# Optimization experiments

Hardware: AMD Instinct MI355X
Metric: run time of the kernel (lower is better)

## Reference

```python
import jax, jax.numpy as jnp
import numpy as np

NUM_CAMERAS = 16
IN_SIZE = 256
OUT_SIZE = 128
BATCH = 8192


def setup_inputs() -> dict:
    key = jax.random.key(0)
    k1, k2, k3, k4 = jax.random.split(key, 4)
    x = jax.random.normal(k1, (BATCH, IN_SIZE), dtype=jnp.float32)
    cam = jax.random.randint(k2, (BATCH,), 0, NUM_CAMERAS, dtype=jnp.int64)
    # Per-camera Linear params, torch-style init U(-1/sqrt(in), 1/sqrt(in))
    bound = 1.0 / np.sqrt(IN_SIZE)
    W = jax.random.uniform(k3, (NUM_CAMERAS, OUT_SIZE, IN_SIZE), dtype=jnp.float32, minval=-bound, maxval=bound)
    b = jax.random.uniform(k4, (NUM_CAMERAS, OUT_SIZE), dtype=jnp.float32, minval=-bound, maxval=bound)
    return {"x": x, "cam": cam, "W": W, "b": b}


def reference(x, cam, W, b):
    # Per-sample expert linear: y_b = W[cam_b] @ x_b + b[cam_b], then sigmoid.
    Wg = W[cam]            # [B, out, in] gathered per-sample weights
    bg = b[cam]            # [B, out]
    y = jnp.einsum('bi,boi->bo', x, Wg) + bg
    return jax.nn.sigmoid(y)
```

## Files before the change

kernel.cpp:

```cpp
#include <hip/hip_runtime.h>
#include <hip/hip_bf16.h>

#define NCAM   16
#define IN     256
#define OUT    128
#define BATCH  8192
#define NSLICE 16
#define SLICE  (BATCH / NSLICE)
#define XPAD   8
#define XROW   (IN + XPAD)

typedef __attribute__((ext_vector_type(8))) short  bfx8;
typedef __attribute__((ext_vector_type(4))) short  bfx4;
typedef __attribute__((ext_vector_type(4))) float  fx4;

__device__ inline short f2bf(float f) {
    __hip_bfloat16 h = __float2bfloat16(f);
    return *reinterpret_cast<short*>(&h);
}

__device__ inline float sigmoidf(float v) {
    return 1.0f / (1.0f + __expf(-v));
}

__global__ __launch_bounds__(256) void fc_expert_kernel(
    const float* __restrict__ x,
    const int*   __restrict__ cam,
    const float* __restrict__ W,
    const float* __restrict__ bias,
    float*       __restrict__ out)
{
    __shared__ int   s_list[SLICE];
    __shared__ int   s_m;
    __shared__ short __align__(16) s_x[16 * XROW];

    const int slice = blockIdx.x;
    const int c     = blockIdx.y;
    const int tid   = threadIdx.x;
    const int lane  = tid & 63;
    const int w     = tid >> 6;
    const int base  = slice * SLICE;

    const int oq   = lane & 15;
    const int quad = lane >> 4;

    if (tid < 64) {
        int cnt = 0;
        for (int i = 0; i < SLICE; i += 64) {
            int g = base + i + lane;
            bool f = (cam[g] == c);
            unsigned long long mask = __ballot(f);
            int pre = __popcll(mask & ((1ull << lane) - 1ull));
            if (f) s_list[cnt + pre] = g;
            cnt += __popcll(mask);
        }
        if (lane == 0) s_m = cnt;
    }

    bfx8 bfrag[2][8];
    #pragma unroll
    for (int t = 0; t < 2; ++t) {
        const int o = w * 32 + t * 16 + oq;
        const float* wrow = W + (size_t)(c * OUT + o) * IN + quad * 8;
        #pragma unroll
        for (int kk = 0; kk < 8; ++kk) {
            fx4 f0 = *(const fx4*)(wrow + kk * 32);
            fx4 f1 = *(const fx4*)(wrow + kk * 32 + 4);
            bfx8 s;
            s[0] = f2bf(f0[0]); s[1] = f2bf(f0[1]); s[2] = f2bf(f0[2]); s[3] = f2bf(f0[3]);
            s[4] = f2bf(f1[0]); s[5] = f2bf(f1[1]); s[6] = f2bf(f1[2]); s[7] = f2bf(f1[3]);
            bfrag[t][kk] = s;
        }
    }
    const float b0 = bias[c * OUT + w * 32 + oq];
    const float b1 = bias[c * OUT + w * 32 + 16 + oq];

    __syncthreads();
    const int m = s_m;

    for (int cb = 0; cb < m; cb += 16) {
        #pragma unroll
        for (int rr = 0; rr < 4; ++rr) {
            int row = rr * 4 + w;
            int li  = cb + row;
            bfx4 sv;
            if (li < m) {
                int g = s_list[li];
                fx4 v = *(const fx4*)(x + (size_t)g * IN + lane * 4);
                sv[0] = f2bf(v[0]); sv[1] = f2bf(v[1]); sv[2] = f2bf(v[2]); sv[3] = f2bf(v[3]);
            } else {
                sv[0] = 0; sv[1] = 0; sv[2] = 0; sv[3] = 0;
            }
            *(bfx4*)(s_x + row * XROW + lane * 4) = sv;
        }
        __syncthreads();

        fx4 acc0 = {0.f, 0.f, 0.f, 0.f};
        fx4 acc1 = {0.f, 0.f, 0.f, 0.f};
        #pragma unroll
        for (int kk = 0; kk < 8; ++kk) {
            bfx8 a = *(const bfx8*)(s_x + oq * XROW + kk * 32 + quad * 8);
            acc0 = __builtin_amdgcn_mfma_f32_16x16x32_bf16(a, bfrag[0][kk], acc0, 0, 0, 0);
            acc1 = __builtin_amdgcn_mfma_f32_16x16x32_bf16(a, bfrag[1][kk], acc1, 0, 0, 0);
        }

        #pragma unroll
        for (int r = 0; r < 4; ++r) {
            int srow = quad * 4 + r;
            if (cb + srow < m) {
                int g = s_list[cb + srow];
                float* op = out + (size_t)g * OUT + w * 32 + oq;
                op[0]  = sigmoidf(acc0[r] + b0);
                op[16] = sigmoidf(acc1[r] + b1);
            }
        }
        __syncthreads();
    }
}

extern "C" void kernel_launch(void* const* d_in, const int* in_sizes, int n_in,
                              void* d_out, int out_size, void* d_ws, size_t ws_size,
                              hipStream_t stream) {
    const float* x    = (const float*)d_in[0];
    const int*   cam  = (const int*)d_in[1];
    const float* W    = (const float*)d_in[2];
    const float* bias = (const float*)d_in[3];
    float* out = (float*)d_out;

    dim3 grid(NSLICE, NCAM);
    fc_expert_kernel<<<grid, 256, 0, stream>>>(x, cam, W, bias, out);
}
```

Baseline: 76.87 us.

## Split output columns across grid z, double slices, parallelize camera scan

Grid grows from 16x16 to 32x16x2 blocks: batch slices are halved and each block handles only 64 of the 128 output columns. Each wave now computes a single MFMA tile. The camera-match scan now uses all four waves with a per-wave count exchanged through shared memory, instead of one wave looping. Weight loads are issued before the scan to overlap latency. This targets low occupancy and the serial scan, at the cost of each x row being loaded and converted twice, once per output half.

```diff
diff --git a/kernel.cpp b/kernel.cpp
--- a/kernel.cpp
+++ b/kernel.cpp
@@ -5,8 +5,9 @@
 #define IN     256
 #define OUT    128
 #define BATCH  8192
-#define NSLICE 16
+#define NSLICE 32
 #define SLICE  (BATCH / NSLICE)
+#define OHALF  64
 #define XPAD   8
 #define XROW   (IN + XPAD)
 
@@ -23,7 +24,7 @@
     return 1.0f / (1.0f + __expf(-v));
 }
 
-__global__ __launch_bounds__(256) void fc_expert_kernel(
+__global__ __launch_bounds__(256, 2) void fc_expert_kernel(
     const float* __restrict__ x,
     const int*   __restrict__ cam,
     const float* __restrict__ W,
@@ -31,11 +32,12 @@
     float*       __restrict__ out)
 {
     __shared__ int   s_list[SLICE];
-    __shared__ int   s_m;
+    __shared__ int   s_cnt[4];
     __shared__ short __align__(16) s_x[16 * XROW];
 
     const int slice = blockIdx.x;
     const int c     = blockIdx.y;
+    const int obase = blockIdx.z * OHALF;
     const int tid   = threadIdx.x;
     const int lane  = tid & 63;
     const int w     = tid >> 6;
@@ -44,39 +46,40 @@
     const int oq   = lane & 15;
     const int quad = lane >> 4;
 
-    if (tid < 64) {
-        int cnt = 0;
-        for (int i = 0; i < SLICE; i += 64) {
-            int g = base + i + lane;
-            bool f = (cam[g] == c);
-            unsigned long long mask = __ballot(f);
-            int pre = __popcll(mask & ((1ull << lane) - 1ull));
-            if (f) s_list[cnt + pre] = g;
-            cnt += __popcll(mask);
-        }
-        if (lane == 0) s_m = cnt;
+    const int g0   = base + w * 64 + lane;
+    const int myc  = cam[g0];
+
+    const int o = obase + w * 16 + oq;
+    const float* wrow = W + (size_t)(c * OUT + o) * IN + quad * 8;
+    fx4 wt[16];
+    #pragma unroll
+    for (int kk = 0; kk < 8; ++kk) {
+        wt[2 * kk]     = *(const fx4*)(wrow + kk * 32);
+        wt[2 * kk + 1] = *(const fx4*)(wrow + kk * 32 + 4);
     }
+    const float bo = bias[c * OUT + o];
 
-    bfx8 bfrag[2][8];
+    const bool f = (myc == c);
+    const unsigned long long mask = __ballot(f);
+    if (lane == 0) s_cnt[w] = __popcll(mask);
+    __syncthreads();
+    int off = 0;
     #pragma unroll
-    for (int t = 0; t < 2; ++t) {
-        const int o = w * 32 + t * 16 + oq;
-        const float* wrow = W + (size_t)(c * OUT + o) * IN + quad * 8;
-        #pragma unroll
-        for (int kk = 0; kk < 8; ++kk) {
-            fx4 f0 = *(const fx4*)(wrow + kk * 32);
-            fx4 f1 = *(const fx4*)(wrow + kk * 32 + 4);
-            bfx8 s;
-            s[0] = f2bf(f0[0]); s[1] = f2bf(f0[1]); s[2] = f2bf(f0[2]); s[3] = f2bf(f0[3]);
-            s[4] = f2bf(f1[0]); s[5] = f2bf(f1[1]); s[6] = f2bf(f1[2]); s[7] = f2bf(f1[3]);
-            bfrag[t][kk] = s;
-        }
+    for (int ww = 0; ww < 4; ++ww) off += (ww < w) ? s_cnt[ww] : 0;
+    const int m = s_cnt[0] + s_cnt[1] + s_cnt[2] + s_cnt[3];
+    const int pre = __popcll(mask & ((1ull << lane) - 1ull));
+    if (f) s_list[off + pre] = g0;
+
+    bfx8 bfrag[8];
+    #pragma unroll
+    for (int kk = 0; kk < 8; ++kk) {
+        fx4 f0 = wt[2 * kk], f1 = wt[2 * kk + 1];
+        bfx8 s;
+        s[0] = f2bf(f0[0]); s[1] = f2bf(f0[1]); s[2] = f2bf(f0[2]); s[3] = f2bf(f0[3]);
+        s[4] = f2bf(f1[0]); s[5] = f2bf(f1[1]); s[6] = f2bf(f1[2]); s[7] = f2bf(f1[3]);
+        bfrag[kk] = s;
     }
-    const float b0 = bias[c * OUT + w * 32 + oq];
-    const float b1 = bias[c * OUT + w * 32 + 16 + oq];
-
     __syncthreads();
-    const int m = s_m;
 
     for (int cb = 0; cb < m; cb += 16) {
         #pragma unroll
@@ -95,13 +98,11 @@
         }
         __syncthreads();
 
-        fx4 acc0 = {0.f, 0.f, 0.f, 0.f};
-        fx4 acc1 = {0.f, 0.f, 0.f, 0.f};
+        fx4 acc = {0.f, 0.f, 0.f, 0.f};
         #pragma unroll
         for (int kk = 0; kk < 8; ++kk) {
             bfx8 a = *(const bfx8*)(s_x + oq * XROW + kk * 32 + quad * 8);
-            acc0 = __builtin_amdgcn_mfma_f32_16x16x32_bf16(a, bfrag[0][kk], acc0, 0, 0, 0);
-            acc1 = __builtin_amdgcn_mfma_f32_16x16x32_bf16(a, bfrag[1][kk], acc1, 0, 0, 0);
+            acc = __builtin_amdgcn_mfma_f32_16x16x32_bf16(a, bfrag[kk], acc, 0, 0, 0);
         }
 
         #pragma unroll
@@ -109,9 +110,7 @@
             int srow = quad * 4 + r;
             if (cb + srow < m) {
                 int g = s_list[cb + srow];
-                float* op = out + (size_t)g * OUT + w * 32 + oq;
-                op[0]  = sigmoidf(acc0[r] + b0);
-                op[16] = sigmoidf(acc1[r] + b1);
+                out[(size_t)g * OUT + o] = sigmoidf(acc[r] + bo);
             }
         }
         __syncthreads();
@@ -127,6 +126,6 @@
     const float* bias = (const float*)d_in[3];
     float* out = (float*)d_out;
 
-    dim3 grid(NSLICE, NCAM);
+    dim3 grid(NSLICE, NCAM, 2);
     fc_expert_kernel<<<grid, 256, 0, stream>>>(x, cam, W, bias, out);
 }
```

After: 74.01 us. -3.7%, faster.

## Bucket samples per camera globally with atomics and tile GEMM over compacted lists

Applied to the files above, without the earlier changes.

Replaces the per-slice ballot scan inside the GEMM kernel with a separate zero pass and an atomic compaction pass that builds a global per-camera index list. The GEMM grid then launches 32-row tiles per camera, and any tile beyond the camera's count exits early. Each block stages the full camera weight matrix in LDS as bf16 and loads x rows directly from global memory into registers, which removes the per-iteration barriers. The cost is two extra kernel launches, atomic contention on 16 counters, and a large grid of mostly empty blocks that still launch.

```diff
diff --git a/kernel.cpp b/kernel.cpp
--- a/kernel.cpp
+++ b/kernel.cpp
@@ -5,14 +5,14 @@
 #define IN     256
 #define OUT    128
 #define BATCH  8192
-#define NSLICE 16
-#define SLICE  (BATCH / NSLICE)
-#define XPAD   8
-#define XROW   (IN + XPAD)
+#define CAP    8192
+#define MT     32
+#define NTILE  (CAP / MT)
+#define XROWW  (IN + 8)
 
-typedef __attribute__((ext_vector_type(8))) short  bfx8;
-typedef __attribute__((ext_vector_type(4))) short  bfx4;
-typedef __attribute__((ext_vector_type(4))) float  fx4;
+typedef short bfx8 __attribute__((ext_vector_type(8)));
+typedef short bfx4 __attribute__((ext_vector_type(4)));
+typedef float fx4  __attribute__((ext_vector_type(4)));
 
 __device__ inline short f2bf(float f) {
     __hip_bfloat16 h = __float2bfloat16(f);
@@ -23,98 +23,94 @@
     return 1.0f / (1.0f + __expf(-v));
 }
 
-__global__ __launch_bounds__(256) void fc_expert_kernel(
+__global__ void zero_cnt_kernel(int* __restrict__ cnt) {
+    if (threadIdx.x < NCAM) cnt[threadIdx.x] = 0;
+}
+
+__global__ void compact_kernel(const int* __restrict__ cam,
+                               int* __restrict__ cnt,
+                               int* __restrict__ list) {
+    int g = blockIdx.x * 256 + threadIdx.x;
+    int c = cam[g];
+    int slot = atomicAdd(&cnt[c], 1);
+    list[c * CAP + slot] = g;
+}
+
+__global__ __launch_bounds__(256, 2) void gemm_kernel(
     const float* __restrict__ x,
-    const int*   __restrict__ cam,
     const float* __restrict__ W,
     const float* __restrict__ bias,
+    const int*   __restrict__ cnt,
+    const int*   __restrict__ list,
     float*       __restrict__ out)
 {
-    __shared__ int   s_list[SLICE];
-    __shared__ int   s_m;
-    __shared__ short __align__(16) s_x[16 * XROW];
+    __shared__ short __align__(16) s_w[OUT * XROWW];
 
-    const int slice = blockIdx.x;
-    const int c     = blockIdx.y;
-    const int tid   = threadIdx.x;
-    const int lane  = tid & 63;
-    const int w     = tid >> 6;
-    const int base  = slice * SLICE;
+    const int t = blockIdx.x;
+    const int c = blockIdx.y;
+    const int m_all = cnt[c];
+    const int base  = t * MT;
+    if (base >= m_all) return;
+    const int m = min(MT, m_all - base);
 
+    const int tid  = threadIdx.x;
+    const int lane = tid & 63;
+    const int w    = tid >> 6;
     const int oq   = lane & 15;
     const int quad = lane >> 4;
 
-    if (tid < 64) {
-        int cnt = 0;
-        for (int i = 0; i < SLICE; i += 64) {
-            int g = base + i + lane;
-            bool f = (cam[g] == c);
-            unsigned long long mask = __ballot(f);
-            int pre = __popcll(mask & ((1ull << lane) - 1ull));
-            if (f) s_list[cnt + pre] = g;
-            cnt += __popcll(mask);
-        }
-        if (lane == 0) s_m = cnt;
-    }
-
-    bfx8 bfrag[2][8];
-    #pragma unroll
-    for (int t = 0; t < 2; ++t) {
-        const int o = w * 32 + t * 16 + oq;
-        const float* wrow = W + (size_t)(c * OUT + o) * IN + quad * 8;
+    {
+        const float* wp = W + (size_t)c * OUT * IN;
         #pragma unroll
-        for (int kk = 0; kk < 8; ++kk) {
-            fx4 f0 = *(const fx4*)(wrow + kk * 32);
-            fx4 f1 = *(const fx4*)(wrow + kk * 32 + 4);
-            bfx8 s;
-            s[0] = f2bf(f0[0]); s[1] = f2bf(f0[1]); s[2] = f2bf(f0[2]); s[3] = f2bf(f0[3]);
-            s[4] = f2bf(f1[0]); s[5] = f2bf(f1[1]); s[6] = f2bf(f1[2]); s[7] = f2bf(f1[3]);
-            bfrag[t][kk] = s;
+        for (int i = 0; i < 32; ++i) {
+            const int row = w * 32 + i;
+            fx4 v = *(const fx4*)(wp + (size_t)row * IN + lane * 4);
+            bfx4 sv;
+            sv[0] = f2bf(v[0]); sv[1] = f2bf(v[1]); sv[2] = f2bf(v[2]); sv[3] = f2bf(v[3]);
+            *(bfx4*)(s_w + row * XROWW + lane * 4) = sv;
         }
     }
     const float b0 = bias[c * OUT + w * 32 + oq];
     const float b1 = bias[c * OUT + w * 32 + 16 + oq];
+    __syncthreads();
 
-    __syncthreads();
-    const int m = s_m;
+    const int* lst = list + c * CAP + base;
 
     for (int cb = 0; cb < m; cb += 16) {
+        const int li = cb + oq;
+        const int g  = lst[min(li, m - 1)];
+        const float* xr = x + (size_t)g * IN + quad * 8;
+        bfx8 afrag[8];
         #pragma unroll
-        for (int rr = 0; rr < 4; ++rr) {
-            int row = rr * 4 + w;
-            int li  = cb + row;
-            bfx4 sv;
-            if (li < m) {
-                int g = s_list[li];
-                fx4 v = *(const fx4*)(x + (size_t)g * IN + lane * 4);
-                sv[0] = f2bf(v[0]); sv[1] = f2bf(v[1]); sv[2] = f2bf(v[2]); sv[3] = f2bf(v[3]);
-            } else {
-                sv[0] = 0; sv[1] = 0; sv[2] = 0; sv[3] = 0;
-            }
-            *(bfx4*)(s_x + row * XROW + lane * 4) = sv;
+        for (int kk = 0; kk < 8; ++kk) {
+            fx4 a0 = *(const fx4*)(xr + kk * 32);
+            fx4 a1 = *(const fx4*)(xr + kk * 32 + 4);
+            bfx8 s;
+            s[0] = f2bf(a0[0]); s[1] = f2bf(a0[1]); s[2] = f2bf(a0[2]); s[3] = f2bf(a0[3]);
+            s[4] = f2bf(a1[0]); s[5] = f2bf(a1[1]); s[6] = f2bf(a1[2]); s[7] = f2bf(a1[3]);
+            afrag[kk] = s;
         }
-        __syncthreads();
 
         fx4 acc0 = {0.f, 0.f, 0.f, 0.f};
         fx4 acc1 = {0.f, 0.f, 0.f, 0.f};
         #pragma unroll
         for (int kk = 0; kk < 8; ++kk) {
-            bfx8 a = *(const bfx8*)(s_x + oq * XROW + kk * 32 + quad * 8);
-            acc0 = __builtin_amdgcn_mfma_f32_16x16x32_bf16(a, bfrag[0][kk], acc0, 0, 0, 0);
-            acc1 = __builtin_amdgcn_mfma_f32_16x16x32_bf16(a, bfrag[1][kk], acc1, 0, 0, 0);
+            bfx8 bv0 = *(const bfx8*)(s_w + (w * 32 + oq) * XROWW + kk * 32 + quad * 8);
+            bfx8 bv1 = *(const bfx8*)(s_w + (w * 32 + 16 + oq) * XROWW + kk * 32 + quad * 8);
+            acc0 = __builtin_amdgcn_mfma_f32_16x16x32_bf16(afrag[kk], bv0, acc0, 0, 0, 0);
+            acc1 = __builtin_amdgcn_mfma_f32_16x16x32_bf16(afrag[kk], bv1, acc1, 0, 0, 0);
         }
 
         #pragma unroll
         for (int r = 0; r < 4; ++r) {
-            int srow = quad * 4 + r;
+            const int srow = quad * 4 + r;
             if (cb + srow < m) {
-                int g = s_list[cb + srow];
-                float* op = out + (size_t)g * OUT + w * 32 + oq;
+                const int gs = lst[cb + srow];
+                float* op = out + (size_t)gs * OUT + w * 32 + oq;
                 op[0]  = sigmoidf(acc0[r] + b0);
                 op[16] = sigmoidf(acc1[r] + b1);
             }
         }
-        __syncthreads();
     }
 }
 
@@ -127,6 +123,11 @@
     const float* bias = (const float*)d_in[3];
     float* out = (float*)d_out;
 
-    dim3 grid(NSLICE, NCAM);
-    fc_expert_kernel<<<grid, 256, 0, stream>>>(x, cam, W, bias, out);
+    int* cnt  = (int*)d_ws;
+    int* list = (int*)((char*)d_ws + 256);
+
+    zero_cnt_kernel<<<1, 64, 0, stream>>>(cnt);
+    compact_kernel<<<BATCH / 256, 256, 0, stream>>>(cam, cnt, list);
+    dim3 grid(NTILE, NCAM);
+    gemm_kernel<<<grid, 256, 0, stream>>>(x, W, bias, cnt, list, out);
 }
```

Result: slower. 104.3 us (+35.7%).
